# Performance work log

Measured on AMD Instinct MI355X. Metric: run time of the kernel, lower is better.

Reference implementation:

```python
import jax, jax.numpy as jnp
import numpy as np

N = 500000   # total atoms
M = 16384    # molecules (superatoms)
D = 256      # fingerprint_dim
EPS_BN = 1e-6
EPS_SM = 1e-8


def setup_inputs() -> dict:
    key = jax.random.key(0)
    ks = jax.random.split(key, 12)
    inp = {}
    inp['superatom'] = jax.random.normal(ks[0], (M, D), dtype=jnp.float32)
    inp['atom'] = jax.random.normal(ks[1], (N, D), dtype=jnp.float32)
    inp['mol_index'] = jnp.sort(jax.random.randint(ks[2], (N,), 0, M, dtype=jnp.int64))
    # align: Linear(2D, 1)
    inp['align_w'] = jax.random.normal(ks[3], (1, 2 * D), dtype=jnp.float32) / np.sqrt(2 * D)
    inp['align_b'] = jnp.zeros((1,), dtype=jnp.float32)
    # attend: LinearBn(D, D) -> linear + BatchNorm1d (eval mode, running stats)
    inp['attend_w'] = jax.random.normal(ks[4], (D, D), dtype=jnp.float32) / np.sqrt(D)
    inp['attend_b'] = jnp.zeros((D,), dtype=jnp.float32)
    inp['bn_gamma'] = jnp.ones((D,), dtype=jnp.float32)
    inp['bn_beta'] = jnp.zeros((D,), dtype=jnp.float32)
    inp['bn_mean'] = 0.01 * jax.random.normal(ks[5], (D,), dtype=jnp.float32)
    inp['bn_var'] = jnp.ones((D,), dtype=jnp.float32) + 0.01 * jax.random.uniform(ks[6], (D,), dtype=jnp.float32)
    # GRUCell(D, D): torch layout, gate order (r, z, n)
    inp['gru_wih'] = jax.random.normal(ks[7], (3 * D, D), dtype=jnp.float32) / np.sqrt(D)
    inp['gru_whh'] = jax.random.normal(ks[8], (3 * D, D), dtype=jnp.float32) / np.sqrt(D)
    inp['gru_bih'] = jnp.zeros((3 * D,), dtype=jnp.float32)
    inp['gru_bhh'] = jnp.zeros((3 * D,), dtype=jnp.float32)
    return inp


def _segment_softmax(x, index, num_segments):
    # x: [N,1], index: [N] -> segment-wise softmax (as in torch_scatter version)
    seg_max = jax.ops.segment_max(x, index, num_segments=num_segments)  # [M,1]
    seg_max = jnp.where(jnp.isfinite(seg_max), seg_max, 0.0)
    e = jnp.exp(x - seg_max[index])
    denom = jax.ops.segment_sum(e, index, num_segments=num_segments)  # [M,1]
    return e / (denom[index] + EPS_SM)


def _gru_cell(x, h, wih, whh, bih, bhh):
    gx = x @ wih.T + bih  # [M,3D]
    gh = h @ whh.T + bhh
    xr, xz, xn = jnp.split(gx, 3, axis=-1)
    hr, hz, hn = jnp.split(gh, 3, axis=-1)
    r = jax.nn.sigmoid(xr + hr)
    z = jax.nn.sigmoid(xz + hz)
    n = jnp.tanh(xn + r * hn)
    return (1.0 - z) * n + z * h


def reference(superatom, atom, mol_index, align_w, align_b, attend_w, attend_b,
              bn_gamma, bn_beta, bn_mean, bn_var, gru_wih, gru_whh, gru_bih, gru_bhh):
    # dropout is identity in eval mode
    superatom_expand = superatom[mol_index]                     # [N,D] gather
    feature_align = jnp.concatenate([superatom_expand, atom], axis=-1)  # [N,2D]
    align_score = jax.nn.leaky_relu(feature_align @ align_w.T + align_b, 0.01)  # [N,1]
    attention_weight = _segment_softmax(align_score, mol_index, M)      # [N,1]
    # attend = Linear + BatchNorm1d (eval)
    attended = atom @ attend_w.T + attend_b
    attended = bn_gamma * (attended - bn_mean) * jax.lax.rsqrt(bn_var + EPS_BN) + bn_beta
    context = jax.ops.segment_sum(attention_weight * attended, mol_index, num_segments=M)  # [M,D]
    context = jax.nn.elu(context)
    update = _gru_cell(context, superatom, gru_wih, gru_whh, gru_bih, gru_bhh)  # [M,D]
    return (update, attention_weight)
```

## Files before the change

### kernel.cpp

```cpp
#include <hip/hip_runtime.h>
#include <hip/hip_bf16.h>

#define D_DIM 256
#define EPS_BN 1e-6f
#define EPS_SM 1e-8f

typedef __bf16 bf16x8 __attribute__((ext_vector_type(8)));
typedef __bf16 bf16x4 __attribute__((ext_vector_type(4)));
typedef float  f32x4  __attribute__((ext_vector_type(4)));

__device__ __forceinline__ float wave_reduce_sum(float v) {
    #pragma unroll
    for (int off = 1; off < 64; off <<= 1) v += __shfl_xor(v, off);
    return v;
}

__device__ __forceinline__ float sigmoidf_(float x) {
    return 1.0f / (1.0f + __expf(-x));
}

__device__ __forceinline__ void cvt_region(const float* __restrict__ s,
                                           __bf16* __restrict__ d,
                                           int n4, int idx, int stride) {
    const float4* s4 = (const float4*)s;
    bf16x4* d4 = (bf16x4*)d;
    for (int i = idx; i < n4; i += stride) {
        float4 v = s4[i];
        bf16x4 o;
        o[0] = (__bf16)v.x; o[1] = (__bf16)v.y; o[2] = (__bf16)v.z; o[3] = (__bf16)v.w;
        d4[i] = o;
    }
}

__global__ __launch_bounds__(256) void k0_convert(
    const float* __restrict__ superatom, __bf16* __restrict__ sup_bf, int M,
    const float* __restrict__ align_w,   const float* __restrict__ align_b,
    float* __restrict__ cvec,
    const int*   __restrict__ mol_index, int* __restrict__ seg_start, int N,
    const float* __restrict__ attend_w,  __bf16* __restrict__ aw_bf,  int n_aw,
    const float* __restrict__ wih,       __bf16* __restrict__ wih_bf, int n_wih,
    const float* __restrict__ whh,       __bf16* __restrict__ whh_bf, int n_whh)
{
    const int tid  = threadIdx.x;
    const int lane = tid & 63;
    const int gw   = (blockIdx.x * 256 + tid) >> 6;
    const int nw   = (gridDim.x * 256) >> 6;

    const float4 w1 = ((const float4*)align_w)[lane];
    const float  b0 = align_b[0];

    for (int m = gw; m < M; m += nw) {
        float4 s = ((const float4*)(superatom + (size_t)m * D_DIM))[lane];
        bf16x4 o;
        o[0] = (__bf16)s.x; o[1] = (__bf16)s.y; o[2] = (__bf16)s.z; o[3] = (__bf16)s.w;
        ((bf16x4*)sup_bf)[(size_t)m * 64 + lane] = o;
        float p = s.x * w1.x + s.y * w1.y + s.z * w1.z + s.w * w1.w;
        p = wave_reduce_sum(p);
        if (lane == 0) cvec[m] = p + b0;
    }

    const int idx    = blockIdx.x * 256 + tid;
    const int stride = gridDim.x * 256;
    cvt_region(attend_w, aw_bf,  n_aw / 4,  idx, stride);
    cvt_region(wih,      wih_bf, n_wih / 4, idx, stride);
    cvt_region(whh,      whh_bf, n_whh / 4, idx, stride);

    for (int i = idx; i < N; i += stride) {
        const int m = mol_index[i];
        if (i == 0) {
            for (int mm = 0; mm <= m; ++mm) seg_start[mm] = 0;
        } else {
            const int mp = mol_index[i - 1];
            if (mp != m)
                for (int mm = mp + 1; mm <= m; ++mm) seg_start[mm] = i;
        }
        if (i == N - 1) {
            for (int mm = m + 1; mm <= M; ++mm) seg_start[mm] = N;
        }
    }
}

__global__ __launch_bounds__(256) void k1_segment(
    const float* __restrict__ atom,
    const float* __restrict__ align_w,
    const float* __restrict__ cvec,
    const int*   __restrict__ seg_start,
    __bf16* __restrict__ ctxwn_bf,
    float* __restrict__ wsum,
    float* __restrict__ att_out,
    int N)
{
    const int m    = blockIdx.x;
    const int tid  = threadIdx.x;
    const int wid  = tid >> 6;
    const int lane = tid & 63;

    const int segs = seg_start[m];
    const int sege = seg_start[m + 1];

    const float cm = cvec[m];
    const float4 wa = ((const float4*)(align_w + D_DIM))[lane];

    __shared__ float smax[4];
    __shared__ float ssum[4];
    __shared__ float sacc[4 * D_DIM];

    float m_run = -3.4e38f;
    float S = 0.0f;
    float4 acc = make_float4(0.f, 0.f, 0.f, 0.f);
    for (int i = segs + wid; i < sege; i += 4) {
        float4 a = ((const float4*)(atom + (size_t)i * D_DIM))[lane];
        float p = a.x * wa.x + a.y * wa.y + a.z * wa.z + a.w * wa.w;
        p = wave_reduce_sum(p);
        float sc = cm + p;
        sc = sc > 0.0f ? sc : 0.01f * sc;
        if (lane == 0) att_out[i] = sc;
        if (sc <= m_run) {
            float e = __expf(sc - m_run);
            S += e;
            acc.x = fmaf(e, a.x, acc.x); acc.y = fmaf(e, a.y, acc.y);
            acc.z = fmaf(e, a.z, acc.z); acc.w = fmaf(e, a.w, acc.w);
        } else {
            float corr = __expf(m_run - sc);
            S = fmaf(S, corr, 1.0f);
            acc.x = fmaf(acc.x, corr, a.x); acc.y = fmaf(acc.y, corr, a.y);
            acc.z = fmaf(acc.z, corr, a.z); acc.w = fmaf(acc.w, corr, a.w);
            m_run = sc;
        }
    }
    if (lane == 0) smax[wid] = m_run;
    __syncthreads();
    const float bmax = fmaxf(fmaxf(smax[0], smax[1]), fmaxf(smax[2], smax[3]));
    {
        float corr = __expf(m_run - bmax);
        S *= corr;
        acc.x *= corr; acc.y *= corr; acc.z *= corr; acc.w *= corr;
    }
    ((float4*)sacc)[wid * 64 + lane] = acc;
    if (lane == 0) ssum[wid] = S;
    __syncthreads();

    const float Stot = ssum[0] + ssum[1] + ssum[2] + ssum[3];
    const float inv  = 1.0f / (Stot + EPS_SM);
    float v = sacc[tid] + sacc[D_DIM + tid] + sacc[2 * D_DIM + tid] + sacc[3 * D_DIM + tid];
    ctxwn_bf[(size_t)m * D_DIM + tid] = (__bf16)(v * inv);
    if (tid == 0) wsum[m] = Stot * inv;

    for (int i = segs + tid; i < sege; i += 256) {
        att_out[i] = __expf(att_out[i] - bmax) * inv;
    }
}

__global__ __launch_bounds__(256) void k2_context(
    const __bf16* __restrict__ A,
    const __bf16* __restrict__ W,
    const float* __restrict__ attend_b,
    const float* __restrict__ gamma_, const float* __restrict__ beta_,
    const float* __restrict__ mean_,  const float* __restrict__ var_,
    const float* __restrict__ wsum,
    __bf16* __restrict__ context_bf)
{
    const int tid  = threadIdx.x;
    const int wid  = tid >> 6;
    const int lane = tid & 63;
    const int quad = lane >> 4;
    const int r16  = lane & 15;
    const int m0   = blockIdx.x * 64;
    const int n0   = blockIdx.y * 64;

    const int arow = m0 + wid * 16 + r16;
    f32x4 acc[4] = {};

    #pragma unroll
    for (int ks = 0; ks < 8; ++ks) {
        const int ko = ks * 32 + quad * 8;
        bf16x8 af = *(const bf16x8*)&A[(size_t)arow * D_DIM + ko];
        #pragma unroll
        for (int t = 0; t < 4; ++t) {
            bf16x8 bf = *(const bf16x8*)&W[(size_t)(n0 + t * 16 + r16) * D_DIM + ko];
            acc[t] = __builtin_amdgcn_mfma_f32_16x16x32_bf16(af, bf, acc[t], 0, 0, 0);
        }
    }

    #pragma unroll
    for (int t = 0; t < 4; ++t) {
        const int col = n0 + t * 16 + r16;
        const float sc = gamma_[col] * rsqrtf(var_[col] + EPS_BN);
        const float cb = (attend_b[col] - mean_[col]) * sc + beta_[col];
        #pragma unroll
        for (int r = 0; r < 4; ++r) {
            const int row = m0 + wid * 16 + quad * 4 + r;
            float pre = acc[t][r] * sc + wsum[row] * cb;
            float e = pre > 0.0f ? pre : (__expf(pre) - 1.0f);
            context_bf[(size_t)row * D_DIM + col] = (__bf16)e;
        }
    }
}

__global__ __launch_bounds__(256) void k3_gru(
    const __bf16* __restrict__ ctx_bf,
    const __bf16* __restrict__ sup_bf,
    const float*  __restrict__ superatom,
    const __bf16* __restrict__ wih_bf,
    const __bf16* __restrict__ whh_bf,
    const float* __restrict__ bih,
    const float* __restrict__ bhh,
    float* __restrict__ out)
{
    const int tid  = threadIdx.x;
    const int wid  = tid >> 6;
    const int lane = tid & 63;
    const int quad = lane >> 4;
    const int r16  = lane & 15;
    const int m0   = blockIdx.x * 64;
    const int n0   = blockIdx.y * 64;

    const int arow = m0 + wid * 16 + r16;
    f32x4 acc[6][4] = {};

    #pragma unroll
    for (int ks = 0; ks < 8; ++ks) {
        const int ko = ks * 32 + quad * 8;
        bf16x8 ca = *(const bf16x8*)&ctx_bf[(size_t)arow * D_DIM + ko];
        bf16x8 ha = *(const bf16x8*)&sup_bf[(size_t)arow * D_DIM + ko];
        #pragma unroll
        for (int t = 0; t < 4; ++t) {
            const int brow = n0 + t * 16 + r16;
            bf16x8 b0 = *(const bf16x8*)&wih_bf[(size_t)(0 * D_DIM + brow) * D_DIM + ko];
            bf16x8 b1 = *(const bf16x8*)&wih_bf[(size_t)(1 * D_DIM + brow) * D_DIM + ko];
            bf16x8 b2 = *(const bf16x8*)&wih_bf[(size_t)(2 * D_DIM + brow) * D_DIM + ko];
            bf16x8 b3 = *(const bf16x8*)&whh_bf[(size_t)(0 * D_DIM + brow) * D_DIM + ko];
            bf16x8 b4 = *(const bf16x8*)&whh_bf[(size_t)(1 * D_DIM + brow) * D_DIM + ko];
            bf16x8 b5 = *(const bf16x8*)&whh_bf[(size_t)(2 * D_DIM + brow) * D_DIM + ko];
            acc[0][t] = __builtin_amdgcn_mfma_f32_16x16x32_bf16(ca, b0, acc[0][t], 0, 0, 0);
            acc[1][t] = __builtin_amdgcn_mfma_f32_16x16x32_bf16(ca, b1, acc[1][t], 0, 0, 0);
            acc[2][t] = __builtin_amdgcn_mfma_f32_16x16x32_bf16(ca, b2, acc[2][t], 0, 0, 0);
            acc[3][t] = __builtin_amdgcn_mfma_f32_16x16x32_bf16(ha, b3, acc[3][t], 0, 0, 0);
            acc[4][t] = __builtin_amdgcn_mfma_f32_16x16x32_bf16(ha, b4, acc[4][t], 0, 0, 0);
            acc[5][t] = __builtin_amdgcn_mfma_f32_16x16x32_bf16(ha, b5, acc[5][t], 0, 0, 0);
        }
    }

    #pragma unroll
    for (int t = 0; t < 4; ++t) {
        const int col = n0 + t * 16 + r16;
        const float br  = bih[col]             + bhh[col];
        const float bz  = bih[D_DIM + col]     + bhh[D_DIM + col];
        const float bxn = bih[2 * D_DIM + col];
        const float bhn = bhh[2 * D_DIM + col];
        #pragma unroll
        for (int r = 0; r < 4; ++r) {
            const int row = m0 + wid * 16 + quad * 4 + r;
            float rg = sigmoidf_(acc[0][t][r] + acc[3][t][r] + br);
            float z  = sigmoidf_(acc[1][t][r] + acc[4][t][r] + bz);
            float n  = tanhf(acc[2][t][r] + bxn + rg * (acc[5][t][r] + bhn));
            float h  = superatom[(size_t)row * D_DIM + col];
            out[(size_t)row * D_DIM + col] = (1.0f - z) * n + z * h;
        }
    }
}

extern "C" void kernel_launch(void* const* d_in, const int* in_sizes, int n_in,
                              void* d_out, int out_size, void* d_ws, size_t ws_size,
                              hipStream_t stream) {
    const float* superatom = (const float*)d_in[0];
    const float* atom      = (const float*)d_in[1];
    const int*   mol_index = (const int*)d_in[2];
    const float* align_w   = (const float*)d_in[3];
    const float* align_b   = (const float*)d_in[4];
    const float* attend_w  = (const float*)d_in[5];
    const float* attend_b  = (const float*)d_in[6];
    const float* bn_gamma  = (const float*)d_in[7];
    const float* bn_beta   = (const float*)d_in[8];
    const float* bn_mean   = (const float*)d_in[9];
    const float* bn_var    = (const float*)d_in[10];
    const float* gru_wih   = (const float*)d_in[11];
    const float* gru_whh   = (const float*)d_in[12];
    const float* gru_bih   = (const float*)d_in[13];
    const float* gru_bhh   = (const float*)d_in[14];

    const int M = in_sizes[0] / D_DIM;
    const int N = in_sizes[2];

    float* out     = (float*)d_out;
    float* att_out = out + (size_t)M * D_DIM;

    char* ws = (char*)d_ws;
    __bf16* ctxwn_bf   = (__bf16*)ws;                     ws += (size_t)M * D_DIM * 2;
    __bf16* context_bf = (__bf16*)ws;                     ws += (size_t)M * D_DIM * 2;
    __bf16* sup_bf     = (__bf16*)ws;                     ws += (size_t)M * D_DIM * 2;
    __bf16* aw_bf      = (__bf16*)ws;                     ws += (size_t)D_DIM * D_DIM * 2;
    __bf16* wih_bf     = (__bf16*)ws;                     ws += (size_t)3 * D_DIM * D_DIM * 2;
    __bf16* whh_bf     = (__bf16*)ws;                     ws += (size_t)3 * D_DIM * D_DIM * 2;
    float*  wsum       = (float*)ws;                      ws += (size_t)M * 4;
    float*  cvec       = (float*)ws;                      ws += (size_t)M * 4;
    int*    seg_start  = (int*)ws;                        ws += (size_t)(M + 1) * 4;

    k0_convert<<<M / 4, 256, 0, stream>>>(superatom, sup_bf, M,
                                          align_w, align_b, cvec,
                                          mol_index, seg_start, N,
                                          attend_w, aw_bf, D_DIM * D_DIM,
                                          gru_wih, wih_bf, 3 * D_DIM * D_DIM,
                                          gru_whh, whh_bf, 3 * D_DIM * D_DIM);
    k1_segment<<<M, 256, 0, stream>>>(atom, align_w, cvec, seg_start,
                                      ctxwn_bf, wsum, att_out, N);
    k2_context<<<dim3(M / 64, D_DIM / 64), 256, 0, stream>>>(ctxwn_bf, aw_bf, attend_b,
                                                             bn_gamma, bn_beta, bn_mean, bn_var,
                                                             wsum, context_bf);
    k3_gru<<<dim3(M / 64, D_DIM / 64), 256, 0, stream>>>(context_bf, sup_bf, superatom,
                                                         wih_bf, whh_bf, gru_bih, gru_bhh,
                                                         out);
}
```

Baseline: 823.1 us.

## Double row tile in context and GRU GEMMs; convert superatom to bf16 in-kernel

The context and GRU GEMM kernels now have each wave compute 32 rows instead of 16. Each loaded weight fragment feeds two MFMAs, so weight traffic per output is halved, and both grids shrink by half. The separate bf16 copy of superatom written in the convert kernel is removed, and the GRU kernel converts fp32 superatom rows to bf16 on the fly. This costs a larger accumulator footprint in the GRU kernel (launch_bounds 256,1, heavy register use, lower occupancy) and double-width fp32 reads of superatom.

Result: no change. 816.9 us (-0.7%).

```diff
diff --git a/kernel.cpp b/kernel.cpp
--- a/kernel.cpp
+++ b/kernel.cpp
@@ -33,7 +33,7 @@
 }
 
 __global__ __launch_bounds__(256) void k0_convert(
-    const float* __restrict__ superatom, __bf16* __restrict__ sup_bf, int M,
+    const float* __restrict__ superatom, int M,
     const float* __restrict__ align_w,   const float* __restrict__ align_b,
     float* __restrict__ cvec,
     const int*   __restrict__ mol_index, int* __restrict__ seg_start, int N,
@@ -51,9 +51,6 @@
 
     for (int m = gw; m < M; m += nw) {
         float4 s = ((const float4*)(superatom + (size_t)m * D_DIM))[lane];
-        bf16x4 o;
-        o[0] = (__bf16)s.x; o[1] = (__bf16)s.y; o[2] = (__bf16)s.z; o[3] = (__bf16)s.w;
-        ((bf16x4*)sup_bf)[(size_t)m * 64 + lane] = o;
         float p = s.x * w1.x + s.y * w1.y + s.z * w1.z + s.w * w1.w;
         p = wave_reduce_sum(p);
         if (lane == 0) cvec[m] = p + b0;
@@ -165,20 +162,24 @@
     const int lane = tid & 63;
     const int quad = lane >> 4;
     const int r16  = lane & 15;
-    const int m0   = blockIdx.x * 64;
+    const int m0   = blockIdx.x * 128;
     const int n0   = blockIdx.y * 64;
 
-    const int arow = m0 + wid * 16 + r16;
-    f32x4 acc[4] = {};
+    const int rowbase = m0 + wid * 32;
+    const int arow0 = rowbase + r16;
+    const int arow1 = rowbase + 16 + r16;
+    f32x4 acc[2][4] = {};
 
     #pragma unroll
     for (int ks = 0; ks < 8; ++ks) {
         const int ko = ks * 32 + quad * 8;
-        bf16x8 af = *(const bf16x8*)&A[(size_t)arow * D_DIM + ko];
+        bf16x8 af0 = *(const bf16x8*)&A[(size_t)arow0 * D_DIM + ko];
+        bf16x8 af1 = *(const bf16x8*)&A[(size_t)arow1 * D_DIM + ko];
         #pragma unroll
         for (int t = 0; t < 4; ++t) {
-            bf16x8 bf = *(const bf16x8*)&W[(size_t)(n0 + t * 16 + r16) * D_DIM + ko];
-            acc[t] = __builtin_amdgcn_mfma_f32_16x16x32_bf16(af, bf, acc[t], 0, 0, 0);
+            bf16x8 bfw = *(const bf16x8*)&W[(size_t)(n0 + t * 16 + r16) * D_DIM + ko];
+            acc[0][t] = __builtin_amdgcn_mfma_f32_16x16x32_bf16(af0, bfw, acc[0][t], 0, 0, 0);
+            acc[1][t] = __builtin_amdgcn_mfma_f32_16x16x32_bf16(af1, bfw, acc[1][t], 0, 0, 0);
         }
     }
 
@@ -188,18 +189,20 @@
         const float sc = gamma_[col] * rsqrtf(var_[col] + EPS_BN);
         const float cb = (attend_b[col] - mean_[col]) * sc + beta_[col];
         #pragma unroll
-        for (int r = 0; r < 4; ++r) {
-            const int row = m0 + wid * 16 + quad * 4 + r;
-            float pre = acc[t][r] * sc + wsum[row] * cb;
-            float e = pre > 0.0f ? pre : (__expf(pre) - 1.0f);
-            context_bf[(size_t)row * D_DIM + col] = (__bf16)e;
-        }
-    }
-}
-
-__global__ __launch_bounds__(256) void k3_gru(
+        for (int g = 0; g < 2; ++g) {
+            #pragma unroll
+            for (int r = 0; r < 4; ++r) {
+                const int row = rowbase + g * 16 + quad * 4 + r;
+                float pre = acc[g][t][r] * sc + wsum[row] * cb;
+                float e = pre > 0.0f ? pre : (__expf(pre) - 1.0f);
+                context_bf[(size_t)row * D_DIM + col] = (__bf16)e;
+            }
+        }
+    }
+}
+
+__global__ __launch_bounds__(256, 1) void k3_gru(
     const __bf16* __restrict__ ctx_bf,
-    const __bf16* __restrict__ sup_bf,
     const float*  __restrict__ superatom,
     const __bf16* __restrict__ wih_bf,
     const __bf16* __restrict__ whh_bf,
@@ -212,17 +215,30 @@
     const int lane = tid & 63;
     const int quad = lane >> 4;
     const int r16  = lane & 15;
-    const int m0   = blockIdx.x * 64;
+    const int m0   = blockIdx.x * 128;
     const int n0   = blockIdx.y * 64;
 
-    const int arow = m0 + wid * 16 + r16;
-    f32x4 acc[6][4] = {};
+    const int rowbase = m0 + wid * 32;
+    const int arow0 = rowbase + r16;
+    const int arow1 = rowbase + 16 + r16;
+
+    f32x4 acc[6][4][2] = {};
 
     #pragma unroll
     for (int ks = 0; ks < 8; ++ks) {
         const int ko = ks * 32 + quad * 8;
-        bf16x8 ca = *(const bf16x8*)&ctx_bf[(size_t)arow * D_DIM + ko];
-        bf16x8 ha = *(const bf16x8*)&sup_bf[(size_t)arow * D_DIM + ko];
+        bf16x8 ca0 = *(const bf16x8*)&ctx_bf[(size_t)arow0 * D_DIM + ko];
+        bf16x8 ca1 = *(const bf16x8*)&ctx_bf[(size_t)arow1 * D_DIM + ko];
+        float4 h0a = *(const float4*)&superatom[(size_t)arow0 * D_DIM + ko];
+        float4 h0b = *(const float4*)&superatom[(size_t)arow0 * D_DIM + ko + 4];
+        float4 h1a = *(const float4*)&superatom[(size_t)arow1 * D_DIM + ko];
+        float4 h1b = *(const float4*)&superatom[(size_t)arow1 * D_DIM + ko + 4];
+        bf16x8 ha0, ha1;
+        ha0[0] = (__bf16)h0a.x; ha0[1] = (__bf16)h0a.y; ha0[2] = (__bf16)h0a.z; ha0[3] = (__bf16)h0a.w;
+        ha0[4] = (__bf16)h0b.x; ha0[5] = (__bf16)h0b.y; ha0[6] = (__bf16)h0b.z; ha0[7] = (__bf16)h0b.w;
+        ha1[0] = (__bf16)h1a.x; ha1[1] = (__bf16)h1a.y; ha1[2] = (__bf16)h1a.z; ha1[3] = (__bf16)h1a.w;
+        ha1[4] = (__bf16)h1b.x; ha1[5] = (__bf16)h1b.y; ha1[6] = (__bf16)h1b.z; ha1[7] = (__bf16)h1b.w;
+
         #pragma unroll
         for (int t = 0; t < 4; ++t) {
             const int brow = n0 + t * 16 + r16;
@@ -232,12 +248,18 @@
             bf16x8 b3 = *(const bf16x8*)&whh_bf[(size_t)(0 * D_DIM + brow) * D_DIM + ko];
             bf16x8 b4 = *(const bf16x8*)&whh_bf[(size_t)(1 * D_DIM + brow) * D_DIM + ko];
             bf16x8 b5 = *(const bf16x8*)&whh_bf[(size_t)(2 * D_DIM + brow) * D_DIM + ko];
-            acc[0][t] = __builtin_amdgcn_mfma_f32_16x16x32_bf16(ca, b0, acc[0][t], 0, 0, 0);
-            acc[1][t] = __builtin_amdgcn_mfma_f32_16x16x32_bf16(ca, b1, acc[1][t], 0, 0, 0);
-            acc[2][t] = __builtin_amdgcn_mfma_f32_16x16x32_bf16(ca, b2, acc[2][t], 0, 0, 0);
-            acc[3][t] = __builtin_amdgcn_mfma_f32_16x16x32_bf16(ha, b3, acc[3][t], 0, 0, 0);
-            acc[4][t] = __builtin_amdgcn_mfma_f32_16x16x32_bf16(ha, b4, acc[4][t], 0, 0, 0);
-            acc[5][t] = __builtin_amdgcn_mfma_f32_16x16x32_bf16(ha, b5, acc[5][t], 0, 0, 0);
+            acc[0][t][0] = __builtin_amdgcn_mfma_f32_16x16x32_bf16(ca0, b0, acc[0][t][0], 0, 0, 0);
+            acc[0][t][1] = __builtin_amdgcn_mfma_f32_16x16x32_bf16(ca1, b0, acc[0][t][1], 0, 0, 0);
+            acc[1][t][0] = __builtin_amdgcn_mfma_f32_16x16x32_bf16(ca0, b1, acc[1][t][0], 0, 0, 0);
+            acc[1][t][1] = __builtin_amdgcn_mfma_f32_16x16x32_bf16(ca1, b1, acc[1][t][1], 0, 0, 0);
+            acc[2][t][0] = __builtin_amdgcn_mfma_f32_16x16x32_bf16(ca0, b2, acc[2][t][0], 0, 0, 0);
+            acc[2][t][1] = __builtin_amdgcn_mfma_f32_16x16x32_bf16(ca1, b2, acc[2][t][1], 0, 0, 0);
+            acc[3][t][0] = __builtin_amdgcn_mfma_f32_16x16x32_bf16(ha0, b3, acc[3][t][0], 0, 0, 0);
+            acc[3][t][1] = __builtin_amdgcn_mfma_f32_16x16x32_bf16(ha1, b3, acc[3][t][1], 0, 0, 0);
+            acc[4][t][0] = __builtin_amdgcn_mfma_f32_16x16x32_bf16(ha0, b4, acc[4][t][0], 0, 0, 0);
+            acc[4][t][1] = __builtin_amdgcn_mfma_f32_16x16x32_bf16(ha1, b4, acc[4][t][1], 0, 0, 0);
+            acc[5][t][0] = __builtin_amdgcn_mfma_f32_16x16x32_bf16(ha0, b5, acc[5][t][0], 0, 0, 0);
+            acc[5][t][1] = __builtin_amdgcn_mfma_f32_16x16x32_bf16(ha1, b5, acc[5][t][1], 0, 0, 0);
         }
     }
 
@@ -249,13 +271,16 @@
         const float bxn = bih[2 * D_DIM + col];
         const float bhn = bhh[2 * D_DIM + col];
         #pragma unroll
-        for (int r = 0; r < 4; ++r) {
-            const int row = m0 + wid * 16 + quad * 4 + r;
-            float rg = sigmoidf_(acc[0][t][r] + acc[3][t][r] + br);
-            float z  = sigmoidf_(acc[1][t][r] + acc[4][t][r] + bz);
-            float n  = tanhf(acc[2][t][r] + bxn + rg * (acc[5][t][r] + bhn));
-            float h  = superatom[(size_t)row * D_DIM + col];
-            out[(size_t)row * D_DIM + col] = (1.0f - z) * n + z * h;
+        for (int g = 0; g < 2; ++g) {
+            #pragma unroll
+            for (int r = 0; r < 4; ++r) {
+                const int row = rowbase + g * 16 + quad * 4 + r;
+                float rg = sigmoidf_(acc[0][t][g][r] + acc[3][t][g][r] + br);
+                float z  = sigmoidf_(acc[1][t][g][r] + acc[4][t][g][r] + bz);
+                float n  = tanhf(acc[2][t][g][r] + bxn + rg * (acc[5][t][g][r] + bhn));
+                float h  = superatom[(size_t)row * D_DIM + col];
+                out[(size_t)row * D_DIM + col] = (1.0f - z) * n + z * h;
+            }
         }
     }
 }
@@ -288,7 +313,6 @@
     char* ws = (char*)d_ws;
     __bf16* ctxwn_bf   = (__bf16*)ws;                     ws += (size_t)M * D_DIM * 2;
     __bf16* context_bf = (__bf16*)ws;                     ws += (size_t)M * D_DIM * 2;
-    __bf16* sup_bf     = (__bf16*)ws;                     ws += (size_t)M * D_DIM * 2;
     __bf16* aw_bf      = (__bf16*)ws;                     ws += (size_t)D_DIM * D_DIM * 2;
     __bf16* wih_bf     = (__bf16*)ws;                     ws += (size_t)3 * D_DIM * D_DIM * 2;
     __bf16* whh_bf     = (__bf16*)ws;                     ws += (size_t)3 * D_DIM * D_DIM * 2;
@@ -296,7 +320,7 @@
     float*  cvec       = (float*)ws;                      ws += (size_t)M * 4;
     int*    seg_start  = (int*)ws;                        ws += (size_t)(M + 1) * 4;
 
-    k0_convert<<<M / 4, 256, 0, stream>>>(superatom, sup_bf, M,
+    k0_convert<<<M / 4, 256, 0, stream>>>(superatom, M,
                                           align_w, align_b, cvec,
                                           mol_index, seg_start, N,
                                           attend_w, aw_bf, D_DIM * D_DIM,
@@ -304,10 +328,10 @@
                                           gru_whh, whh_bf, 3 * D_DIM * D_DIM);
     k1_segment<<<M, 256, 0, stream>>>(atom, align_w, cvec, seg_start,
                                       ctxwn_bf, wsum, att_out, N);
-    k2_context<<<dim3(M / 64, D_DIM / 64), 256, 0, stream>>>(ctxwn_bf, aw_bf, attend_b,
-                                                             bn_gamma, bn_beta, bn_mean, bn_var,
-                                                             wsum, context_bf);
-    k3_gru<<<dim3(M / 64, D_DIM / 64), 256, 0, stream>>>(context_bf, sup_bf, superatom,
-                                                         wih_bf, whh_bf, gru_bih, gru_bhh,
-                                                         out);
-}
+    k2_context<<<dim3(M / 128, D_DIM / 64), 256, 0, stream>>>(ctxwn_bf, aw_bf, attend_b,
+                                                              bn_gamma, bn_beta, bn_mean, bn_var,
+                                                              wsum, context_bf);
+    k3_gru<<<dim3(M / 128, D_DIM / 64), 256, 0, stream>>>(context_bf, superatom,
+                                                          wih_bf, whh_bf, gru_bih, gru_bhh,
+                                                          out);
+}
```
